# Kernel tuning notes

Hardware: AMD Instinct MI355X
Metric: run time of the kernel (lower is better)

## Reference

```python
import jax, jax.numpy as jnp
import numpy as np

DEPTH = 4
HEADS = 8
WINDOW = 256
RPW = 2                      # relay_tokens_per_window
SEQ_PER_RELAY = WINDOW // RPW  # 128 tokens per relay group
RELAY_START = 2              # depth_start_relay_attn (1-indexed layer number)
LN_EPS = 1e-5


def setup_inputs() -> dict:
    key = jax.random.key(0)
    ks = jax.random.split(key, 8)
    b, t, d, dff = 2, 2048, 512, 2048
    s = 0.02
    return {
        "x": jax.random.normal(ks[0], (b, t, d), dtype=jnp.float32),
        "relay_emb": jax.random.normal(ks[1], (1, d), dtype=jnp.float32) * s,
        "ln1_g": jnp.ones((DEPTH, d), jnp.float32),
        "ln1_b": jnp.zeros((DEPTH, d), jnp.float32),
        "loc_qkv_w": jax.random.normal(ks[2], (DEPTH, d, 3 * d), dtype=jnp.float32) * s,
        "loc_out_w": jax.random.normal(ks[3], (DEPTH, d, d), dtype=jnp.float32) * s,
        "loc_out_b": jnp.zeros((DEPTH, d), jnp.float32),
        "glob_qkv_w": jax.random.normal(ks[4], (DEPTH, d, 3 * d), dtype=jnp.float32) * s,
        "glob_out_w": jax.random.normal(ks[5], (DEPTH, d, d), dtype=jnp.float32) * s,
        "glob_out_b": jnp.zeros((DEPTH, d), jnp.float32),
        "ln2_g": jnp.ones((DEPTH, d), jnp.float32),
        "ln2_b": jnp.zeros((DEPTH, d), jnp.float32),
        "ff_w1": jax.random.normal(ks[6], (DEPTH, d, dff), dtype=jnp.float32) * s,
        "ff_b1": jnp.zeros((DEPTH, dff), jnp.float32),
        "ff_w2": jax.random.normal(ks[7], (DEPTH, dff, d), dtype=jnp.float32) * s,
        "ff_b2": jnp.zeros((DEPTH, d), jnp.float32),
    }


def _layernorm(x, g, b):
    m = jnp.mean(x, axis=-1, keepdims=True)
    v = jnp.mean(jnp.square(x - m), axis=-1, keepdims=True)
    return (x - m) * jax.lax.rsqrt(v + LN_EPS) * g + b


def _self_attention(x, qkv_w, out_w, out_b):
    # full (non-causal) multi-head attention, as in FullAttention
    b, t, d = x.shape
    h, dh = HEADS, d // HEADS
    q, k, v = jnp.split(x @ qkv_w, 3, axis=-1)
    mh = lambda u: u.reshape(b, t, h, dh).transpose(0, 2, 1, 3)  # b h t dh
    q, k, v = mh(q), mh(k), mh(v)
    dots = jnp.einsum('bhid,bhjd->bhij', q, k) * (dh ** -0.5)
    attn = jax.nn.softmax(dots, axis=-1)
    o = jnp.einsum('bhij,bhjd->bhid', attn, v)
    o = o.transpose(0, 2, 1, 3).reshape(b, t, d)
    return o @ out_w + out_b


def reference(x, relay_emb, ln1_g, ln1_b, loc_qkv_w, loc_out_w, loc_out_b,
              glob_qkv_w, glob_out_w, glob_out_b, ln2_g, ln2_b,
              ff_w1, ff_b1, ff_w2, ff_b2):
    b, t, d = x.shape
    # insert one relay token every SEQ_PER_RELAY tokens
    x = x.reshape(b, -1, SEQ_PER_RELAY, d)
    G = x.shape[1]
    rel = jnp.broadcast_to(relay_emb[None, None], (b, G, 1, d))
    x = jnp.concatenate([rel, x], axis=2).reshape(b, -1, d)  # (b, G*(129), d)

    for l in range(DEPTH):
        # attention block: PreNorm -> AttentionLayer, residual from sequence wrapper
        y = _layernorm(x, ln1_g[l], ln1_b[l])
        if (l + 1) >= RELAY_START:
            y = y.reshape(b, G, SEQ_PER_RELAY + 1, d)
            r = y[:, :, 0]                                       # (b, G, d) relay tokens
            r = _self_attention(r, glob_qkv_w[l], glob_out_w[l], glob_out_b[l]) + r
            y = jnp.concatenate([r[:, :, None], y[:, :, 1:]], axis=2).reshape(b, -1, d)
        x = x + _self_attention(y, loc_qkv_w[l], loc_out_w[l], loc_out_b[l])
        # feedforward block: PreNorm -> FFN with LeakyReLU(0.01)
        z = _layernorm(x, ln2_g[l], ln2_b[l])
        z = jax.nn.leaky_relu(z @ ff_w1[l] + ff_b1[l], negative_slope=0.01) @ ff_w2[l] + ff_b2[l]
        x = x + z

    # strip relay tokens
    x = x.reshape(b, G, SEQ_PER_RELAY + 1, d)
    return x[:, :, 1:].reshape(b, -1, d)
```

## Files before the change

### kernel.cpp

```cpp
#include <hip/hip_runtime.h>

typedef __attribute__((ext_vector_type(8))) __bf16 bf16x8;
typedef __attribute__((ext_vector_type(8))) unsigned short u16x8;
typedef __attribute__((ext_vector_type(4))) unsigned short u16x4;
typedef __attribute__((ext_vector_type(2))) unsigned int u32x2;
typedef __attribute__((ext_vector_type(4))) float f32x4;
typedef unsigned short u16;
typedef unsigned int u32;

#define TSEQ 2064
#define NTOK 4128

__device__ __forceinline__ float bf2f(u16 u) {
  unsigned x = ((unsigned)u) << 16;
  return __builtin_bit_cast(float, x);
}
__device__ __forceinline__ u16 f2bf(float f) {
  unsigned u = __builtin_bit_cast(unsigned, f);
  u += 0x7fffu + ((u >> 16) & 1u);
  return (u16)(u >> 16);
}

__device__ __forceinline__ void gll16(const u16* g, u16* l) {
  __builtin_amdgcn_global_load_lds((const __attribute__((address_space(1))) void*)g,
                                   (__attribute__((address_space(3))) void*)l, 16, 0, 0);
}
__device__ __forceinline__ int swz(int row, int col) {
  return row * 64 + (col ^ ((row & 7) << 3));
}

__global__ __launch_bounds__(256) void transpose_all(
    const float* __restrict__ s0, const float* __restrict__ s1,
    const float* __restrict__ s2, const float* __restrict__ s3,
    const float* __restrict__ s4, const float* __restrict__ s5,
    u16* __restrict__ d0, u16* __restrict__ d1, u16* __restrict__ d2,
    u16* __restrict__ d3, u16* __restrict__ d4, u16* __restrict__ d5)
{
  __shared__ float tile[32][33];
  int bid = blockIdx.x;
  const float* src; u16* dst; int K, N, r;
  if (bid < 6144)       { int w = bid >> 11 >= 1 && bid >= 3072; r = bid - (bid >= 3072 ? 3072 : 0);
                          K = 512; N = 1536; src = bid >= 3072 ? s1 : s0; dst = bid >= 3072 ? d1 : d0; }
  else if (bid < 8192)  { r = bid - (bid >= 7168 ? 7168 : 6144);
                          K = 512; N = 512;  src = bid >= 7168 ? s3 : s2; dst = bid >= 7168 ? d3 : d2; }
  else if (bid < 12288) { r = bid - 8192;  K = 512;  N = 2048; src = s4; dst = d4; }
  else                  { r = bid - 12288; K = 2048; N = 512;  src = s5; dst = d5; }
  const int tx = N >> 5, per = tx * (K >> 5);
  const int l = r / per; r -= l * per;
  const int n0 = (r % tx) * 32, k0 = (r / tx) * 32;
  src += (size_t)l * K * N;
  dst += (size_t)l * K * N;
  const int c = threadIdx.x & 31, rr0 = threadIdx.x >> 5;
#pragma unroll
  for (int rr = rr0; rr < 32; rr += 8)
    tile[rr][c] = src[(size_t)(k0 + rr) * N + n0 + c];
  __syncthreads();
#pragma unroll
  for (int rr = rr0; rr < 32; rr += 8)
    dst[(size_t)(n0 + rr) * K + k0 + c] = f2bf(tile[c][rr]);
}

__global__ void build_x(const float* __restrict__ xin, const float* __restrict__ relay,
                        float* __restrict__ xw)
{
  const int total = 2 * TSEQ * 512;
  for (int idx = blockIdx.x * 256 + threadIdx.x; idx < total; idx += gridDim.x * 256) {
    int col = idx & 511;
    int tok = (idx >> 9) % TSEQ;
    int b   = idx / (TSEQ * 512);
    int g = tok / 129, s = tok % 129;
    float v = (s == 0) ? relay[col]
                       : xin[((size_t)b * 2048 + g * 128 + (s - 1)) * 512 + col];
    xw[idx] = v;
  }
}

__global__ void extract_out(const float* __restrict__ xw, float* __restrict__ out)
{
  const int total = 2 * 2048 * 512;
  for (int idx = blockIdx.x * 256 + threadIdx.x; idx < total; idx += gridDim.x * 256) {
    int col = idx & 511;
    int tok = (idx >> 9) & 2047;
    int b   = idx / (2048 * 512);
    int g = tok >> 7, s = tok & 127;
    out[idx] = xw[((size_t)b * TSEQ + g * 129 + s + 1) * 512 + col];
  }
}

__global__ __launch_bounds__(256) void ln_kernel(const float* __restrict__ x,
                                                 const float* __restrict__ g,
                                                 const float* __restrict__ bta,
                                                 u16* __restrict__ y, int M)
{
  const int wid = threadIdx.x >> 6, lane = threadIdx.x & 63;
  const int row = blockIdx.x * 4 + wid;
  if (row >= M) return;
  const float* xr = x + (size_t)row * 512;
  float v[8];
  float s = 0.f;
#pragma unroll
  for (int j = 0; j < 8; ++j) { v[j] = xr[j * 64 + lane]; s += v[j]; }
#pragma unroll
  for (int m = 1; m <= 32; m <<= 1) s += __shfl_xor(s, m);
  float mean = s * (1.f / 512.f);
  float vs = 0.f;
#pragma unroll
  for (int j = 0; j < 8; ++j) { float d = v[j] - mean; vs += d * d; }
#pragma unroll
  for (int m = 1; m <= 32; m <<= 1) vs += __shfl_xor(vs, m);
  float rstd = rsqrtf(vs * (1.f / 512.f) + 1e-5f);
  u16* yr = y + (size_t)row * 512;
#pragma unroll
  for (int j = 0; j < 8; ++j) {
    int c = j * 64 + lane;
    yr[c] = f2bf((v[j] - mean) * rstd * g[c] + bta[c]);
  }
}

__device__ __forceinline__ int relay_tok(int r) {
  return (r >> 4) * TSEQ + (r & 15) * 129;
}

template<bool HAS_BIAS, bool ACT, bool RESID, bool OUT_BF16, bool VOUT,
         bool RELAYA, bool RELAYC>
__global__ __launch_bounds__(256, 4) void gemm3(
    const u16* __restrict__ A, const u16* __restrict__ Bt,
    const float* __restrict__ bias, const float* __restrict__ resid,
    void* __restrict__ outp, u16* __restrict__ vgout, int M, int N, int K)
{
  __shared__ __attribute__((aligned(16))) u16 As[128 * 64];
  __shared__ __attribute__((aligned(16))) u16 Bs[128 * 64];
  const int tid = threadIdx.x, lane = tid & 63, wid = tid >> 6;
  const int row0 = blockIdx.x * 128, col0 = blockIdx.y * 128;
  const int wm = (wid >> 1) * 64, wn = (wid & 1) * 64;
  const int srow = tid >> 3, sseg = tid & 7;
  f32x4 acc[4][4];
#pragma unroll
  for (int m = 0; m < 4; ++m)
#pragma unroll
    for (int n = 0; n < 4; ++n) acc[m][n] = (f32x4)0.f;
  const u16* Bb = Bt + (size_t)col0 * K;
  const int fr = lane & 15, g = lane >> 4;

  for (int k0 = 0; k0 < K; k0 += 64) {
    __syncthreads();
#pragma unroll
    for (int i = 0; i < 4; ++i) {
      int row = srow + i * 32, ss = sseg ^ (row & 7);
      size_t arow = RELAYA ? (size_t)relay_tok(row & 31) : (size_t)(row0 + row);
      gll16(A + arow * K + k0 + ss * 8, &As[row * 64 + sseg * 8]);
      gll16(Bb + (size_t)row * K + k0 + ss * 8, &Bs[row * 64 + sseg * 8]);
    }
    __syncthreads();
#pragma unroll
    for (int kk = 0; kk < 2; ++kk) {
      bf16x8 a[4], bb[4];
#pragma unroll
      for (int m = 0; m < 4; ++m) a[m] = *(const bf16x8*)&As[swz(wm + m * 16 + fr, kk * 32 + g * 8)];
#pragma unroll
      for (int n = 0; n < 4; ++n) bb[n] = *(const bf16x8*)&Bs[swz(wn + n * 16 + fr, kk * 32 + g * 8)];
      __builtin_amdgcn_s_setprio(1);
#pragma unroll
      for (int m = 0; m < 4; ++m)
#pragma unroll
        for (int n = 0; n < 4; ++n)
          acc[m][n] = __builtin_amdgcn_mfma_f32_16x16x32_bf16(a[m], bb[n], acc[m][n], 0, 0, 0);
      __builtin_amdgcn_s_setprio(0);
    }
  }

#pragma unroll
  for (int m = 0; m < 4; ++m) {
#pragma unroll
    for (int n = 0; n < 4; ++n) {
#pragma unroll
      for (int j = 0; j < 4; ++j) {
        int grow = row0 + wm + m * 16 + g * 4 + j;
        int gcol = col0 + wn + n * 16 + fr;
        if (grow < M) {
          float v = acc[m][n][j];
          if (HAS_BIAS) v += bias[gcol];
          if (ACT) v = (v > 0.f) ? v : 0.01f * v;
          if (RESID) v += resid[(size_t)grow * N + gcol];
          if (RELAYC) {
            u16* p = (u16*)outp + (size_t)relay_tok(grow) * 512 + gcol;
            *p = f2bf(v + bf2f(*p));
          } else if (VOUT && gcol >= 1024) {
            int hh = (gcol - 1024) >> 6, dd = gcol & 63;
            int bb2 = grow >= TSEQ;
            int tok = grow - bb2 * TSEQ;
            vgout[((size_t)((bb2 * 8 + hh) * 64 + dd)) * 2112 + tok] = f2bf(v);
          } else if (OUT_BF16) {
            if (VOUT && gcol < 512) v *= 0.125f;
            ((u16*)outp)[(size_t)grow * N + gcol] = f2bf(v);
          } else {
            ((float*)outp)[(size_t)grow * N + gcol] = v;
          }
        }
      }
    }
  }
}

__global__ __launch_bounds__(512, 4) void flash_attn4(const u16* __restrict__ big,
                                                      const u16* __restrict__ vg,
                                                      u16* __restrict__ op0,
                                                      u16* __restrict__ op1,
                                                      float2* __restrict__ mlb)
{
  __shared__ __attribute__((aligned(16))) u16 Qs[128 * 64];
  __shared__ __attribute__((aligned(16))) u16 Ks[2][64 * 64];
  __shared__ __attribute__((aligned(16))) u16 Vs[2][64 * 64];
  const int tid = threadIdx.x, lane = tid & 63, wid = tid >> 6;
  const int qt = blockIdx.x, bh = blockIdx.y, z = blockIdx.z;
  const int b = bh >> 3, h = bh & 7;
  const int q0 = qt * 128;
  const int srow = tid >> 3, sseg = tid & 7;
  const int ktbeg = z * 17, ktend = z ? 33 : 17;

  const u16* kb = big + ((size_t)(b * TSEQ)) * 1536 + h * 64 + 512;
  const u16* vb = vg + (size_t)bh * 64 * 2112;
#pragma unroll
  for (int i = 0; i < 2; ++i) {
    int row = srow + i * 64;
    int grow = b * TSEQ + q0 + row; grow = grow < NTOK ? grow : NTOK - 1;
    int ss = sseg ^ (row & 7);
    gll16(big + (size_t)grow * 1536 + h * 64 + ss * 8, &Qs[row * 64 + sseg * 8]);
  }
  {
    int ss = sseg ^ (srow & 7);
    gll16(kb + (size_t)(ktbeg * 64 + srow) * 1536 + ss * 8, &Ks[0][srow * 64 + sseg * 8]);
    gll16(vb + (size_t)srow * 2112 + ktbeg * 64 + ss * 8, &Vs[0][srow * 64 + sseg * 8]);
  }
  __syncthreads();
  const int fr = lane & 15, g = lane >> 4;
  bf16x8 aq0 = *(const bf16x8*)&Qs[swz(wid * 16 + fr, g * 8)];
  bf16x8 aq1 = *(const bf16x8*)&Qs[swz(wid * 16 + fr, 32 + g * 8)];
  u16* Pw = &Qs[wid * 1024];

  f32x4 oacc[4];
#pragma unroll
  for (int nf = 0; nf < 4; ++nf) oacc[nf] = (f32x4)0.f;
  float mrow = -1e30f, lsum = 0.f;
  int cur = 0;

  for (int kt = ktbeg; kt < ktend; ++kt) {
    if (kt + 1 < ktend) {
      int ss = sseg ^ (srow & 7);
      gll16(kb + (size_t)((kt + 1) * 64 + srow) * 1536 + ss * 8, &Ks[cur ^ 1][srow * 64 + sseg * 8]);
      gll16(vb + (size_t)srow * 2112 + (kt + 1) * 64 + ss * 8, &Vs[cur ^ 1][srow * 64 + sseg * 8]);
    }
    const u16* ks = &Ks[cur][0];
    const u16* vs = &Vs[cur][0];
    f32x4 s[4];
    __builtin_amdgcn_s_setprio(1);
#pragma unroll
    for (int n = 0; n < 4; ++n) {
      int row = n * 16 + fr;
      bf16x8 ak0 = *(const bf16x8*)&ks[swz(row, g * 8)];
      bf16x8 ak1 = *(const bf16x8*)&ks[swz(row, 32 + g * 8)];
      f32x4 t = (f32x4)0.f;
      t = __builtin_amdgcn_mfma_f32_16x16x32_bf16(ak0, aq0, t, 0, 0, 0);
      t = __builtin_amdgcn_mfma_f32_16x16x32_bf16(ak1, aq1, t, 0, 0, 0);
      s[n] = t;
    }
    __builtin_amdgcn_s_setprio(0);
    if (kt == 32) {
#pragma unroll
      for (int n = 0; n < 4; ++n) {
        int kbase = kt * 64 + n * 16 + g * 4;
#pragma unroll
        for (int j = 0; j < 4; ++j)
          if (kbase + j >= TSEQ) s[n][j] = -1e30f;
      }
    }
    float mloc = s[0][0];
#pragma unroll
    for (int n = 0; n < 4; ++n)
#pragma unroll
      for (int j = 0; j < 4; ++j) mloc = fmaxf(mloc, s[n][j]);
    mloc = fmaxf(mloc, __shfl_xor(mloc, 16));
    mloc = fmaxf(mloc, __shfl_xor(mloc, 32));
    if (!__all(mloc <= mrow + 8.f)) {
      float nm = fmaxf(mrow, mloc);
      float sc = __expf(mrow - nm);
      mrow = nm;
      lsum *= sc;
      float s4[4];
#pragma unroll
      for (int j = 0; j < 4; ++j) s4[j] = __shfl(sc, g * 4 + j);
#pragma unroll
      for (int nf = 0; nf < 4; ++nf)
#pragma unroll
        for (int j = 0; j < 4; ++j) oacc[nf][j] *= s4[j];
    }
    float psum = 0.f;
#pragma unroll
    for (int n = 0; n < 4; ++n) {
      float p0 = __expf(s[n][0] - mrow), p1 = __expf(s[n][1] - mrow);
      float p2 = __expf(s[n][2] - mrow), p3 = __expf(s[n][3] - mrow);
      psum += (p0 + p1) + (p2 + p3);
      u32x2 pk;
      pk[0] = __builtin_amdgcn_perm(__builtin_bit_cast(u32, p1), __builtin_bit_cast(u32, p0), 0x07060302u);
      pk[1] = __builtin_amdgcn_perm(__builtin_bit_cast(u32, p3), __builtin_bit_cast(u32, p2), 0x07060302u);
      *(u32x2*)&Pw[swz(fr, n * 16 + g * 4)] = pk;
    }
    psum += __shfl_xor(psum, 16);
    psum += __shfl_xor(psum, 32);
    lsum += psum;
    __builtin_amdgcn_s_setprio(1);
#pragma unroll
    for (int kc = 0; kc < 2; ++kc) {
      bf16x8 ap = *(const bf16x8*)&Pw[swz(fr, kc * 32 + g * 8)];
#pragma unroll
      for (int nf = 0; nf < 4; ++nf) {
        bf16x8 bv = *(const bf16x8*)&vs[swz(nf * 16 + fr, kc * 32 + g * 8)];
        oacc[nf] = __builtin_amdgcn_mfma_f32_16x16x32_bf16(ap, bv, oacc[nf], 0, 0, 0);
      }
    }
    __builtin_amdgcn_s_setprio(0);
    __syncthreads();
    cur ^= 1;
  }

  u16* op = z ? op1 : op0;
#pragma unroll
  for (int nf = 0; nf < 4; ++nf) {
#pragma unroll
    for (int j = 0; j < 4; ++j) {
      int row = q0 + wid * 16 + g * 4 + j;
      if (row < TSEQ)
        op[((size_t)(b * TSEQ + row)) * 512 + h * 64 + nf * 16 + fr] = f2bf(oacc[nf][j]);
    }
  }
  if (lane < 16) {
    int row = q0 + wid * 16 + fr;
    if (row < TSEQ)
      mlb[(size_t)(z * 16 + bh) * 2112 + row] = float2{mrow, lsum};
  }
}

__global__ __launch_bounds__(256) void fa_combine(const u16* __restrict__ op0,
                                                  const u16* __restrict__ op1,
                                                  const float2* __restrict__ mlb,
                                                  u16* __restrict__ ob)
{
  int idx = blockIdx.x * 256 + threadIdx.x;
  int tok = idx >> 7;
  int c4 = (idx & 127) * 4;
  int b = tok >= TSEQ;
  int row = tok - b * TSEQ;
  int h = c4 >> 6;
  float2 ml0 = mlb[(size_t)(b * 8 + h) * 2112 + row];
  float2 ml1 = mlb[(size_t)(16 + b * 8 + h) * 2112 + row];
  float M = fmaxf(ml0.x, ml1.x);
  float a0 = __expf(ml0.x - M), a1 = __expf(ml1.x - M);
  float inv = 1.f / (ml0.y * a0 + ml1.y * a1);
  u16x4 v0 = *(const u16x4*)&op0[(size_t)tok * 512 + c4];
  u16x4 v1 = *(const u16x4*)&op1[(size_t)tok * 512 + c4];
  u16x4 o;
#pragma unroll
  for (int j = 0; j < 4; ++j)
    o[j] = f2bf((bf2f(v0[j]) * a0 + bf2f(v1[j]) * a1) * inv);
  *(u16x4*)&ob[(size_t)tok * 512 + c4] = o;
}

__global__ __launch_bounds__(256) void global_attn(const u16* __restrict__ rqkv,
                                                   u16* __restrict__ ro)
{
  const int b = blockIdx.x >> 3, h = blockIdx.x & 7;
  __shared__ float q[16][64], k[16][64], v[16][64], s[16][16], p[16][16];
  const int tid = threadIdx.x;
  for (int idx = tid; idx < 1024; idx += 256) {
    int rr = idx >> 6, c = idx & 63;
    size_t base = (size_t)(b * 16 + rr) * 1536 + h * 64 + c;
    q[rr][c] = bf2f(rqkv[base]);
    k[rr][c] = bf2f(rqkv[base + 512]);
    v[rr][c] = bf2f(rqkv[base + 1024]);
  }
  __syncthreads();
  {
    int i = tid >> 4, j = tid & 15;
    float acc = 0.f;
#pragma unroll
    for (int d = 0; d < 64; ++d) acc += q[i][d] * k[j][d];
    s[i][j] = acc * 0.125f;
  }
  __syncthreads();
  if (tid < 16) {
    float mx = -1e30f;
#pragma unroll
    for (int j = 0; j < 16; ++j) mx = fmaxf(mx, s[tid][j]);
    float sum = 0.f;
#pragma unroll
    for (int j = 0; j < 16; ++j) { float e = __expf(s[tid][j] - mx); p[tid][j] = e; sum += e; }
    float iv = 1.f / sum;
#pragma unroll
    for (int j = 0; j < 16; ++j) p[tid][j] *= iv;
  }
  __syncthreads();
  for (int idx = tid; idx < 1024; idx += 256) {
    int rr = idx >> 6, c = idx & 63;
    float acc = 0.f;
#pragma unroll
    for (int j = 0; j < 16; ++j) acc += p[rr][j] * v[j][c];
    ro[(size_t)(b * 16 + rr) * 512 + h * 64 + c] = f2bf(acc);
  }
}

extern "C" void kernel_launch(void* const* d_in, const int* in_sizes, int n_in,
                              void* d_out, int out_size, void* d_ws, size_t ws_size,
                              hipStream_t stream)
{
  const float* x_in     = (const float*)d_in[0];
  const float* rel_emb  = (const float*)d_in[1];
  const float* ln1_g    = (const float*)d_in[2];
  const float* ln1_b    = (const float*)d_in[3];
  const float* loc_qkv  = (const float*)d_in[4];
  const float* loc_ow   = (const float*)d_in[5];
  const float* loc_ob   = (const float*)d_in[6];
  const float* glob_qkv = (const float*)d_in[7];
  const float* glob_ow  = (const float*)d_in[8];
  const float* glob_ob  = (const float*)d_in[9];
  const float* ln2_g    = (const float*)d_in[10];
  const float* ln2_b    = (const float*)d_in[11];
  const float* ff_w1    = (const float*)d_in[12];
  const float* ff_b1    = (const float*)d_in[13];
  const float* ff_w2    = (const float*)d_in[14];
  const float* ff_b2    = (const float*)d_in[15];

  char* ws = (char*)d_ws;
  float*  xbuf = (float*)(ws + 0);
  u16*    ybuf = (u16*)(ws + 8650752);
  u16*    obuf = (u16*)(ws + 12976128);
  u16*    big  = (u16*)(ws + 17301504);
  u16*    vg   = (u16*)(ws + 34603008);
  u16*    wLQ  = (u16*)(ws + 38928384);
  u16*    wGQ  = (u16*)(ws + 45219840);
  u16*    wLO  = (u16*)(ws + 51511296);
  u16*    wGO  = (u16*)(ws + 53608448);
  u16*    wF1  = (u16*)(ws + 55705600);
  u16*    wF2  = (u16*)(ws + 64094208);
  u16*    rqkv = (u16*)(ws + 72482816);
  u16*    rov  = (u16*)(ws + 72581120);
  float2* mlb  = (float2*)(ws + 72712192);

  dim3 B(256);
  transpose_all<<<16384, B, 0, stream>>>(loc_qkv, glob_qkv, loc_ow, glob_ow, ff_w1, ff_w2,
                                         wLQ, wGQ, wLO, wGO, wF1, wF2);
  build_x<<<8256, B, 0, stream>>>(x_in, rel_emb, xbuf);

  for (int l = 0; l < 4; ++l) {
    ln_kernel<<<1032, B, 0, stream>>>(xbuf, ln1_g + l * 512, ln1_b + l * 512, ybuf, NTOK);
    if (l + 1 >= 2) {
      gemm3<false, false, false, true, false, true, false><<<dim3(1, 12), B, 0, stream>>>(
          ybuf, wGQ + (size_t)l * 1536 * 512, nullptr, nullptr, rqkv, nullptr, 32, 1536, 512);
      global_attn<<<16, B, 0, stream>>>(rqkv, rov);
      gemm3<true, false, false, true, false, false, true><<<dim3(1, 4), B, 0, stream>>>(
          rov, wGO + (size_t)l * 512 * 512, glob_ob + l * 512, nullptr, ybuf, nullptr, 32, 512, 512);
    }
    gemm3<false, false, false, true, true, false, false><<<dim3(33, 12), B, 0, stream>>>(
        ybuf, wLQ + (size_t)l * 1536 * 512, nullptr, nullptr, big, vg, NTOK, 1536, 512);
    flash_attn4<<<dim3(17, 16, 2), dim3(512), 0, stream>>>(big, vg, ybuf, obuf, mlb);
    fa_combine<<<2064, B, 0, stream>>>(ybuf, obuf, mlb, obuf);
    gemm3<true, false, true, false, false, false, false><<<dim3(33, 4), B, 0, stream>>>(
        obuf, wLO + (size_t)l * 512 * 512, loc_ob + l * 512, xbuf, xbuf, nullptr, NTOK, 512, 512);
    ln_kernel<<<1032, B, 0, stream>>>(xbuf, ln2_g + l * 512, ln2_b + l * 512, ybuf, NTOK);
    gemm3<true, true, false, true, false, false, false><<<dim3(33, 16), B, 0, stream>>>(
        ybuf, wF1 + (size_t)l * 2048 * 512, ff_b1 + l * 2048, nullptr, big, nullptr, NTOK, 2048, 512);
    gemm3<true, false, true, false, false, false, false><<<dim3(33, 4), B, 0, stream>>>(
        big, wF2 + (size_t)l * 512 * 2048, ff_b2 + l * 512, xbuf, xbuf, nullptr, NTOK, 512, 2048);
  }
  extract_out<<<8192, B, 0, stream>>>(xbuf, (float*)d_out);
}
```

Measured before the change: 931.9 us.

## Double-buffer GEMM LDS loads, add split-K atomics and XCD-aware block remap

The GEMM kernel now double-buffers its LDS tiles, issuing the next K-slice's global-to-LDS loads while MFMAs run on the current one, which removes one barrier per iteration. The residual-producing GEMMs (attention out-projection and FF2) use split-K over a z grid dimension and accumulate into the fp32 residual buffer with atomicAdd, which raises block count for these narrow N=512 outputs. Large GEMMs also remap block IDs so that neighbouring tiles land on the same XCD for better L2 reuse. In exchange, LDS use doubles, which may limit occupancy, and the atomics add nondeterministic summation order and extra memory traffic.

```diff
diff --git a/kernel.cpp b/kernel.cpp
--- a/kernel.cpp
+++ b/kernel.cpp
@@ -39,7 +39,7 @@
   __shared__ float tile[32][33];
   int bid = blockIdx.x;
   const float* src; u16* dst; int K, N, r;
-  if (bid < 6144)       { int w = bid >> 11 >= 1 && bid >= 3072; r = bid - (bid >= 3072 ? 3072 : 0);
+  if (bid < 6144)       { r = bid - (bid >= 3072 ? 3072 : 0);
                           K = 512; N = 1536; src = bid >= 3072 ? s1 : s0; dst = bid >= 3072 ? d1 : d0; }
   else if (bid < 8192)  { r = bid - (bid >= 7168 ? 7168 : 6144);
                           K = 512; N = 512;  src = bid >= 7168 ? s3 : s2; dst = bid >= 7168 ? d3 : d2; }
@@ -121,44 +121,63 @@
   return (r >> 4) * TSEQ + (r & 15) * 129;
 }
 
-template<bool HAS_BIAS, bool ACT, bool RESID, bool OUT_BF16, bool VOUT,
-         bool RELAYA, bool RELAYC>
-__global__ __launch_bounds__(256, 4) void gemm3(
+template<bool HAS_BIAS, bool ACT, bool OUT_BF16, bool VOUT,
+         bool RELAYA, bool RELAYC, bool ATOMIC, bool SWZGRID>
+__global__ __launch_bounds__(256, 4) void gemm4(
     const u16* __restrict__ A, const u16* __restrict__ Bt,
-    const float* __restrict__ bias, const float* __restrict__ resid,
-    void* __restrict__ outp, u16* __restrict__ vgout, int M, int N, int K)
-{
-  __shared__ __attribute__((aligned(16))) u16 As[128 * 64];
-  __shared__ __attribute__((aligned(16))) u16 Bs[128 * 64];
+    const float* __restrict__ bias, void* __restrict__ outp,
+    u16* __restrict__ vgout, int M, int N, int K, int Kb)
+{
+  __shared__ __attribute__((aligned(16))) u16 As[2][128 * 64];
+  __shared__ __attribute__((aligned(16))) u16 Bs[2][128 * 64];
   const int tid = threadIdx.x, lane = tid & 63, wid = tid >> 6;
-  const int row0 = blockIdx.x * 128, col0 = blockIdx.y * 128;
+  int brow, bcol;
+  if (SWZGRID) {
+    int nrow = gridDim.x, ncol = gridDim.y;
+    int nb = nrow * ncol;
+    int lin = blockIdx.y * nrow + blockIdx.x;
+    int q = nb >> 3, r = nb & 7;
+    int xcd = lin & 7, i = lin >> 3;
+    int wg = (xcd < r ? xcd * (q + 1) : r * (q + 1) + (xcd - r) * q) + i;
+    brow = wg / ncol; bcol = wg % ncol;
+  } else { brow = blockIdx.x; bcol = blockIdx.y; }
+  const int row0 = brow * 128, col0 = bcol * 128;
+  const int kbeg = blockIdx.z * Kb, kend = kbeg + Kb;
   const int wm = (wid >> 1) * 64, wn = (wid & 1) * 64;
   const int srow = tid >> 3, sseg = tid & 7;
+  const int fr = lane & 15, g = lane >> 4;
   f32x4 acc[4][4];
 #pragma unroll
   for (int m = 0; m < 4; ++m)
 #pragma unroll
     for (int n = 0; n < 4; ++n) acc[m][n] = (f32x4)0.f;
   const u16* Bb = Bt + (size_t)col0 * K;
-  const int fr = lane & 15, g = lane >> 4;
-
-  for (int k0 = 0; k0 < K; k0 += 64) {
-    __syncthreads();
-#pragma unroll
-    for (int i = 0; i < 4; ++i) {
-      int row = srow + i * 32, ss = sseg ^ (row & 7);
-      size_t arow = RELAYA ? (size_t)relay_tok(row & 31) : (size_t)(row0 + row);
-      gll16(A + arow * K + k0 + ss * 8, &As[row * 64 + sseg * 8]);
-      gll16(Bb + (size_t)row * K + k0 + ss * 8, &Bs[row * 64 + sseg * 8]);
-    }
-    __syncthreads();
+
+#define STAGE(buf, kk0)                                                        \
+  {                                                                            \
+    _Pragma("unroll")                                                          \
+    for (int i = 0; i < 4; ++i) {                                              \
+      int row = srow + i * 32, ss = sseg ^ (row & 7);                          \
+      size_t arow = RELAYA ? (size_t)relay_tok(row & 31) : (size_t)(row0 + row); \
+      gll16(A + arow * K + (kk0) + ss * 8, &As[buf][row * 64 + sseg * 8]);     \
+      gll16(Bb + (size_t)row * K + (kk0) + ss * 8, &Bs[buf][row * 64 + sseg * 8]); \
+    }                                                                          \
+  }
+
+  STAGE(0, kbeg);
+  __syncthreads();
+  int cur = 0;
+  for (int k0 = kbeg; k0 < kend; k0 += 64) {
+    if (k0 + 64 < kend) STAGE(cur ^ 1, k0 + 64);
+    const u16* as_ = &As[cur][0];
+    const u16* bs_ = &Bs[cur][0];
 #pragma unroll
     for (int kk = 0; kk < 2; ++kk) {
       bf16x8 a[4], bb[4];
 #pragma unroll
-      for (int m = 0; m < 4; ++m) a[m] = *(const bf16x8*)&As[swz(wm + m * 16 + fr, kk * 32 + g * 8)];
-#pragma unroll
-      for (int n = 0; n < 4; ++n) bb[n] = *(const bf16x8*)&Bs[swz(wn + n * 16 + fr, kk * 32 + g * 8)];
+      for (int m = 0; m < 4; ++m) a[m] = *(const bf16x8*)&as_[swz(wm + m * 16 + fr, kk * 32 + g * 8)];
+#pragma unroll
+      for (int n = 0; n < 4; ++n) bb[n] = *(const bf16x8*)&bs_[swz(wn + n * 16 + fr, kk * 32 + g * 8)];
       __builtin_amdgcn_s_setprio(1);
 #pragma unroll
       for (int m = 0; m < 4; ++m)
@@ -167,7 +186,10 @@
           acc[m][n] = __builtin_amdgcn_mfma_f32_16x16x32_bf16(a[m], bb[n], acc[m][n], 0, 0, 0);
       __builtin_amdgcn_s_setprio(0);
     }
-  }
+    __syncthreads();
+    cur ^= 1;
+  }
+#undef STAGE
 
 #pragma unroll
   for (int m = 0; m < 4; ++m) {
@@ -179,9 +201,8 @@
         int gcol = col0 + wn + n * 16 + fr;
         if (grow < M) {
           float v = acc[m][n][j];
-          if (HAS_BIAS) v += bias[gcol];
+          if (HAS_BIAS && (!ATOMIC || blockIdx.z == 0)) v += bias[gcol];
           if (ACT) v = (v > 0.f) ? v : 0.01f * v;
-          if (RESID) v += resid[(size_t)grow * N + gcol];
           if (RELAYC) {
             u16* p = (u16*)outp + (size_t)relay_tok(grow) * 512 + gcol;
             *p = f2bf(v + bf2f(*p));
@@ -190,6 +211,8 @@
             int bb2 = grow >= TSEQ;
             int tok = grow - bb2 * TSEQ;
             vgout[((size_t)((bb2 * 8 + hh) * 64 + dd)) * 2112 + tok] = f2bf(v);
+          } else if (ATOMIC) {
+            atomicAdd((float*)outp + (size_t)grow * N + gcol, v);
           } else if (OUT_BF16) {
             if (VOUT && gcol < 512) v *= 0.125f;
             ((u16*)outp)[(size_t)grow * N + gcol] = f2bf(v);
@@ -453,23 +476,23 @@
   for (int l = 0; l < 4; ++l) {
     ln_kernel<<<1032, B, 0, stream>>>(xbuf, ln1_g + l * 512, ln1_b + l * 512, ybuf, NTOK);
     if (l + 1 >= 2) {
-      gemm3<false, false, false, true, false, true, false><<<dim3(1, 12), B, 0, stream>>>(
-          ybuf, wGQ + (size_t)l * 1536 * 512, nullptr, nullptr, rqkv, nullptr, 32, 1536, 512);
+      gemm4<false, false, true, false, true, false, false, false><<<dim3(1, 12, 1), B, 0, stream>>>(
+          ybuf, wGQ + (size_t)l * 1536 * 512, nullptr, rqkv, nullptr, 32, 1536, 512, 512);
       global_attn<<<16, B, 0, stream>>>(rqkv, rov);
-      gemm3<true, false, false, true, false, false, true><<<dim3(1, 4), B, 0, stream>>>(
-          rov, wGO + (size_t)l * 512 * 512, glob_ob + l * 512, nullptr, ybuf, nullptr, 32, 512, 512);
-    }
-    gemm3<false, false, false, true, true, false, false><<<dim3(33, 12), B, 0, stream>>>(
-        ybuf, wLQ + (size_t)l * 1536 * 512, nullptr, nullptr, big, vg, NTOK, 1536, 512);
+      gemm4<true, false, true, false, false, true, false, false><<<dim3(1, 4, 1), B, 0, stream>>>(
+          rov, wGO + (size_t)l * 512 * 512, glob_ob + l * 512, ybuf, nullptr, 32, 512, 512, 512);
+    }
+    gemm4<false, false, true, true, false, false, false, true><<<dim3(33, 12, 1), B, 0, stream>>>(
+        ybuf, wLQ + (size_t)l * 1536 * 512, nullptr, big, vg, NTOK, 1536, 512, 512);
     flash_attn4<<<dim3(17, 16, 2), dim3(512), 0, stream>>>(big, vg, ybuf, obuf, mlb);
     fa_combine<<<2064, B, 0, stream>>>(ybuf, obuf, mlb, obuf);
-    gemm3<true, false, true, false, false, false, false><<<dim3(33, 4), B, 0, stream>>>(
-        obuf, wLO + (size_t)l * 512 * 512, loc_ob + l * 512, xbuf, xbuf, nullptr, NTOK, 512, 512);
+    gemm4<true, false, false, false, false, false, true, true><<<dim3(33, 4, 4), B, 0, stream>>>(
+        obuf, wLO + (size_t)l * 512 * 512, loc_ob + l * 512, xbuf, nullptr, NTOK, 512, 512, 128);
     ln_kernel<<<1032, B, 0, stream>>>(xbuf, ln2_g + l * 512, ln2_b + l * 512, ybuf, NTOK);
-    gemm3<true, true, false, true, false, false, false><<<dim3(33, 16), B, 0, stream>>>(
-        ybuf, wF1 + (size_t)l * 2048 * 512, ff_b1 + l * 2048, nullptr, big, nullptr, NTOK, 2048, 512);
-    gemm3<true, false, true, false, false, false, false><<<dim3(33, 4), B, 0, stream>>>(
-        big, wF2 + (size_t)l * 512 * 2048, ff_b2 + l * 512, xbuf, xbuf, nullptr, NTOK, 512, 2048);
+    gemm4<true, true, true, false, false, false, false, true><<<dim3(33, 16, 1), B, 0, stream>>>(
+        ybuf, wF1 + (size_t)l * 2048 * 512, ff_b1 + l * 2048, big, nullptr, NTOK, 2048, 512, 512);
+    gemm4<true, false, false, false, false, false, true, true><<<dim3(33, 4, 4), B, 0, stream>>>(
+        big, wF2 + (size_t)l * 512 * 2048, ff_b2 + l * 512, xbuf, nullptr, NTOK, 512, 2048, 512);
   }
   extract_out<<<8192, B, 0, stream>>>(xbuf, (float*)d_out);
 }
```

After: 1.070 ms. 1.15x slower.
